# Optimization experiments

Measured on AMD Instinct MI355X. Metric: run time of the kernel, lower is better.

Reference implementation:

```python
import jax, jax.numpy as jnp
import numpy as np

D_MODEL = 1024
N_HEADS = 16
D_K = D_MODEL // N_HEADS
D_FF = 4096
EPS = 1e-5


def layer_norm(x, g, b):
    mu = jnp.mean(x, axis=-1, keepdims=True)
    var = jnp.var(x, axis=-1, keepdims=True)
    return (x - mu) * jax.lax.rsqrt(var + EPS) * g + b


def setup_inputs() -> dict:
    key = jax.random.key(0)
    ks = jax.random.split(key, 16)
    B, S = 4, 2048
    s_in = 1.0 / np.sqrt(D_MODEL)
    s_ff = 1.0 / np.sqrt(D_FF)
    return {
        "x": jax.random.normal(ks[0], (B, S, D_MODEL), jnp.float32),
        "mask": jnp.ones((B, 1, 1, S), jnp.int32),
        "Wq": jax.random.normal(ks[1], (D_MODEL, D_MODEL), jnp.float32) * s_in,
        "bq": jnp.zeros((D_MODEL,), jnp.float32),
        "Wk": jax.random.normal(ks[2], (D_MODEL, D_MODEL), jnp.float32) * s_in,
        "bk": jnp.zeros((D_MODEL,), jnp.float32),
        "Wv": jax.random.normal(ks[3], (D_MODEL, D_MODEL), jnp.float32) * s_in,
        "bv": jnp.zeros((D_MODEL,), jnp.float32),
        "Wo": jax.random.normal(ks[4], (D_MODEL, D_MODEL), jnp.float32) * s_in,
        "bo": jnp.zeros((D_MODEL,), jnp.float32),
        "W1": jax.random.normal(ks[5], (D_MODEL, D_FF), jnp.float32) * s_in,
        "b1": jnp.zeros((D_FF,), jnp.float32),
        "W2": jax.random.normal(ks[6], (D_FF, D_MODEL), jnp.float32) * s_ff,
        "b2": jnp.zeros((D_MODEL,), jnp.float32),
        "ln1_g": jnp.ones((D_MODEL,), jnp.float32),
        "ln1_b": jnp.zeros((D_MODEL,), jnp.float32),
        "ln2_g": jnp.ones((D_MODEL,), jnp.float32),
        "ln2_b": jnp.zeros((D_MODEL,), jnp.float32),
    }


def reference(x, mask, Wq, bq, Wk, bk, Wv, bv, Wo, bo, W1, b1, W2, b2,
              ln1_g, ln1_b, ln2_g, ln2_b):
    B, S, _ = x.shape
    h = layer_norm(x, ln1_g, ln1_b)  # norm1(x), used for q/k/v
    # project and split heads: [B,S,D] -> [B,H,S,Dk]
    def heads(t):
        return t.reshape(B, S, N_HEADS, D_K).transpose(0, 2, 1, 3)
    Q = heads(h @ Wq + bq)
    K = heads(h @ Wk + bk)
    V = heads(h @ Wv + bv)
    scores = jnp.einsum('bhqd,bhkd->bhqk', Q, K) / jnp.sqrt(jnp.float32(D_K))
    scores = jnp.where(mask == 0, jnp.float32(-1e9), scores)
    attn = jax.nn.softmax(scores, axis=-1)
    out = jnp.einsum('bhqk,bhkd->bhqd', attn, V)
    out = out.transpose(0, 2, 1, 3).reshape(B, S, D_MODEL)
    attn_out = out @ Wo + bo
    x = x + attn_out
    # FFN with pre-norm (torch nn.GELU default = exact erf gelu)
    h2 = layer_norm(x, ln2_g, ln2_b)
    ff = jax.nn.gelu(h2 @ W1 + b1, approximate=False) @ W2 + b2
    return x + ff
```

## Files before the change

kernel.cpp:

```cpp
#include <hip/hip_runtime.h>
#include <stdint.h>
#include <string.h>


typedef unsigned int       u32;
typedef unsigned short     u16;
typedef __bf16 bf16x8 __attribute__((ext_vector_type(8)));
typedef float  floatx4 __attribute__((ext_vector_type(4)));

#define D_MODEL 1024
#define N_HEADS 16
#define D_K     64
#define D_FF    4096
#define S_LEN   2048
#define N_TOK   8192
#define LDQKV   3072

__device__ __forceinline__ u16 f2b(float f) {
    u32 u = __float_as_uint(f);
    u32 r = (u + 0x7fffu + ((u >> 16) & 1u)) >> 16;
    return (u16)r;
}

__device__ __forceinline__ void gl_lds16(const void* g, void* l) {
    __builtin_amdgcn_global_load_lds(
        (const __attribute__((address_space(1))) u32*)g,
        (__attribute__((address_space(3))) u32*)l, 16, 0, 0);
}

__global__ __launch_bounds__(256) void transpose_bf16_kernel(
    const float* __restrict__ src, u16* __restrict__ dst, int R, int C)
{
    __shared__ float tile[32][33];
    int cb = blockIdx.x * 32, rb = blockIdx.y * 32;
    int tx = threadIdx.x & 31, ty = threadIdx.x >> 5;
    #pragma unroll
    for (int yy = ty; yy < 32; yy += 8)
        tile[yy][tx] = src[(size_t)(rb + yy) * C + cb + tx];
    __syncthreads();
    #pragma unroll
    for (int yy = ty; yy < 32; yy += 8)
        dst[(size_t)(cb + yy) * R + rb + tx] = f2b(tile[tx][yy]);
}

__global__ __launch_bounds__(256) void vt_kernel(
    const u16* __restrict__ Qkv, u16* __restrict__ Vt)
{
    __shared__ u32 tile[64 * 65];
    int b = blockIdx.z, h = blockIdx.y, s0 = blockIdx.x * 64;
    int t = threadIdx.x;
    int r = t >> 2, cg = (t & 3) * 16;
    const u16* src = &Qkv[((size_t)(b * S_LEN + s0 + r)) * LDQKV + 2048 + h * D_K + cg];
    uint4 a0 = *(const uint4*)src;
    uint4 a1 = *(const uint4*)(src + 8);
    u16 vals[16];
    memcpy(vals, &a0, 16); memcpy(vals + 8, &a1, 16);
    #pragma unroll
    for (int j = 0; j < 16; j++) tile[r * 65 + cg + j] = vals[j];
    __syncthreads();
    int f = t & 63, w = t >> 6;
    u16 outv[16];
    #pragma unroll
    for (int j = 0; j < 16; j++) outv[j] = (u16)tile[(w * 16 + j) * 65 + f];
    uint4 o0, o1; memcpy(&o0, outv, 16); memcpy(&o1, outv + 8, 16);
    u16* dst = &Vt[((size_t)((b * N_HEADS + h) * D_K + f)) * S_LEN + s0 + w * 16];
    *(uint4*)dst = o0; *(uint4*)(dst + 8) = o1;
}

__global__ __launch_bounds__(256) void ln_kernel(
    const float* __restrict__ x, const float* __restrict__ g,
    const float* __restrict__ b, u16* __restrict__ out)
{
    int row = blockIdx.x;
    int t = threadIdx.x;
    const float4* xr = reinterpret_cast<const float4*>(x + (size_t)row * D_MODEL);
    float4 v = xr[t];
    float s  = v.x + v.y + v.z + v.w;
    float ss = v.x * v.x + v.y * v.y + v.z * v.z + v.w * v.w;
    #pragma unroll
    for (int off = 32; off >= 1; off >>= 1) {
        s  += __shfl_down(s,  off);
        ss += __shfl_down(ss, off);
    }
    __shared__ float red[8];
    int wid = t >> 6, ln = t & 63;
    if (ln == 0) { red[wid] = s; red[4 + wid] = ss; }
    __syncthreads();
    float S  = red[0] + red[1] + red[2] + red[3];
    float SS = red[4] + red[5] + red[6] + red[7];
    float mu  = S * (1.0f / D_MODEL);
    float var = SS * (1.0f / D_MODEL) - mu * mu;
    float rs  = rsqrtf(var + 1e-5f);
    const float4* g4 = reinterpret_cast<const float4*>(g);
    const float4* b4 = reinterpret_cast<const float4*>(b);
    float4 gv = g4[t], bv = b4[t];
    float y0 = (v.x - mu) * rs * gv.x + bv.x;
    float y1 = (v.y - mu) * rs * gv.y + bv.y;
    float y2 = (v.z - mu) * rs * gv.z + bv.z;
    float y3 = (v.w - mu) * rs * gv.w + bv.w;
    uint2 pk;
    pk.x = (u32)f2b(y0) | ((u32)f2b(y1) << 16);
    pk.y = (u32)f2b(y2) | ((u32)f2b(y3) << 16);
    *reinterpret_cast<uint2*>(out + (size_t)row * D_MODEL + t * 4) = pk;
}

__global__ __launch_bounds__(256) void gemm_bt(
    const u16* __restrict__ A, const u16* __restrict__ Bt,
    const float* __restrict__ bias, const float* __restrict__ biasK,
    const float* __restrict__ biasV, const float* __restrict__ resid,
    float* __restrict__ outF, u16* __restrict__ outB,
    int M, int N, int K, int flags)
{
    __shared__ u16 As[128 * 32];
    __shared__ u16 Bs[128 * 32];
    int m0 = blockIdx.y * 128, n0 = blockIdx.x * 128;
    int t = threadIdx.x;
    int wave = t >> 6, lane = t & 63, quad = lane >> 4, lr = lane & 15;
    int wm = (wave >> 1) * 64, wn = (wave & 1) * 64;

    floatx4 acc[4][4] = {};

    int seg0 = t;
    int r0 = seg0 >> 2, c0 = (seg0 & 3) * 8;
    int seg1 = t + 256;
    int r1 = seg1 >> 2, c1 = (seg1 & 3) * 8;

    for (int k0 = 0; k0 < K; k0 += 32) {
        gl_lds16(&A [(size_t)(m0 + r0) * K + k0 + c0], &As[seg0 * 8]);
        gl_lds16(&A [(size_t)(m0 + r1) * K + k0 + c1], &As[seg1 * 8]);
        gl_lds16(&Bt[(size_t)(n0 + r0) * K + k0 + c0], &Bs[seg0 * 8]);
        gl_lds16(&Bt[(size_t)(n0 + r1) * K + k0 + c1], &Bs[seg1 * 8]);
        __syncthreads();

        bf16x8 af[4], bfr[4];
        #pragma unroll
        for (int mt = 0; mt < 4; mt++)
            af[mt] = *reinterpret_cast<const bf16x8*>(&As[(wm + mt * 16 + lr) * 32 + quad * 8]);
        #pragma unroll
        for (int nt = 0; nt < 4; nt++)
            bfr[nt] = *reinterpret_cast<const bf16x8*>(&Bs[(wn + nt * 16 + lr) * 32 + quad * 8]);
        #pragma unroll
        for (int mt = 0; mt < 4; mt++)
            #pragma unroll
            for (int nt = 0; nt < 4; nt++)
                acc[mt][nt] = __builtin_amdgcn_mfma_f32_16x16x32_bf16(
                    af[mt], bfr[nt], acc[mt][nt], 0, 0, 0);
        __syncthreads();
    }

    bool do_gelu = (flags & 1) != 0;
    #pragma unroll
    for (int mt = 0; mt < 4; mt++) {
        #pragma unroll
        for (int nt = 0; nt < 4; nt++) {
            int c = n0 + wn + nt * 16 + lr;
            float bsv;
            if (biasK) {
                if (c >= 2048)      bsv = biasV[c - 2048];
                else if (c >= 1024) bsv = biasK[c - 1024];
                else                bsv = bias[c];
            } else {
                bsv = bias[c];
            }
            #pragma unroll
            for (int i = 0; i < 4; i++) {
                int r = m0 + wm + mt * 16 + quad * 4 + i;
                float v = acc[mt][nt][i] + bsv;
                if (resid) v += resid[(size_t)r * N + c];
                if (do_gelu) v = 0.5f * v * (1.0f + erff(v * 0.70710678118654752f));
                if (outF) outF[(size_t)r * N + c] = v;
                if (outB) outB[(size_t)r * N + c] = f2b(v);
            }
        }
    }
}

__global__ __launch_bounds__(256, 4) void attn_mfma_kernel(
    const u16* __restrict__ Qkv, const u16* __restrict__ Vt,
    const int* __restrict__ mask, u16* __restrict__ ctx)
{
    __shared__ u16 Ks[64 * 72];
    __shared__ u16 Vs[64 * 72];
    __shared__ u16 Ps[128 * 72];
    __shared__ float Ms[64];

    int b = blockIdx.z, h = blockIdx.y;
    int q0 = blockIdx.x * 128;
    int t = threadIdx.x;
    int wave = t >> 6, lane = t & 63, quad = lane >> 4, lr = lane & 15;
    int wm = wave * 32;

    bf16x8 qf[2][2];
    #pragma unroll
    for (int mt = 0; mt < 2; mt++)
        #pragma unroll
        for (int kk = 0; kk < 2; kk++)
            qf[mt][kk] = *(const bf16x8*)&Qkv[((size_t)(b * S_LEN + q0 + wm + mt * 16 + lr)) * LDQKV
                                              + h * D_K + kk * 32 + quad * 8];

    floatx4 o[2][4] = {};
    float lsum[2][4] = {};
    const float scale = 0.125f;

    for (int kt = 0; kt < S_LEN / 64; kt++) {
        __syncthreads();
        {
            int row = t >> 2, cg = (t & 3) * 16;
            const u16* kg = &Qkv[((size_t)(b * S_LEN + kt * 64 + row)) * LDQKV + 1024 + h * D_K + cg];
            *(uint4*)&Ks[row * 72 + cg]     = *(const uint4*)kg;
            *(uint4*)&Ks[row * 72 + cg + 8] = *(const uint4*)(kg + 8);
            const u16* vg = &Vt[((size_t)((b * N_HEADS + h) * D_K + row)) * S_LEN + kt * 64 + cg];
            *(uint4*)&Vs[row * 72 + cg]     = *(const uint4*)vg;
            *(uint4*)&Vs[row * 72 + cg + 8] = *(const uint4*)(vg + 8);
            if (t < 64) Ms[t] = (mask[b * S_LEN + kt * 64 + t] == 0) ? -1e9f : 0.0f;
        }
        __syncthreads();

        floatx4 s[2][4] = {};
        #pragma unroll
        for (int kk = 0; kk < 2; kk++) {
            bf16x8 bk[4];
            #pragma unroll
            for (int n = 0; n < 4; n++)
                bk[n] = *(const bf16x8*)&Ks[(n * 16 + lr) * 72 + kk * 32 + quad * 8];
            #pragma unroll
            for (int mt = 0; mt < 2; mt++)
                #pragma unroll
                for (int n = 0; n < 4; n++)
                    s[mt][n] = __builtin_amdgcn_mfma_f32_16x16x32_bf16(
                        qf[mt][kk], bk[n], s[mt][n], 0, 0, 0);
        }

        #pragma unroll
        for (int mt = 0; mt < 2; mt++) {
            #pragma unroll
            for (int n = 0; n < 4; n++) {
                float msk = Ms[n * 16 + lr];
                #pragma unroll
                for (int i = 0; i < 4; i++) {
                    float p = __expf(s[mt][n][i] * scale + msk);
                    lsum[mt][i] += p;
                    Ps[(wm + mt * 16 + quad * 4 + i) * 72 + n * 16 + lr] = f2b(p);
                }
            }
        }

        bf16x8 bv[4][2];
        #pragma unroll
        for (int kk = 0; kk < 2; kk++)
            #pragma unroll
            for (int n = 0; n < 4; n++)
                bv[n][kk] = *(const bf16x8*)&Vs[(n * 16 + lr) * 72 + kk * 32 + quad * 8];

        __syncthreads();

        #pragma unroll
        for (int kk = 0; kk < 2; kk++) {
            #pragma unroll
            for (int mt = 0; mt < 2; mt++) {
                bf16x8 ap = *(const bf16x8*)&Ps[(wm + mt * 16 + lr) * 72 + kk * 32 + quad * 8];
                #pragma unroll
                for (int n = 0; n < 4; n++)
                    o[mt][n] = __builtin_amdgcn_mfma_f32_16x16x32_bf16(
                        ap, bv[n][kk], o[mt][n], 0, 0, 0);
            }
        }
    }

    #pragma unroll
    for (int mt = 0; mt < 2; mt++)
        #pragma unroll
        for (int i = 0; i < 4; i++) {
            float v = lsum[mt][i];
            v += __shfl_xor(v, 1);
            v += __shfl_xor(v, 2);
            v += __shfl_xor(v, 4);
            v += __shfl_xor(v, 8);
            lsum[mt][i] = 1.0f / v;
        }
    #pragma unroll
    for (int mt = 0; mt < 2; mt++)
        #pragma unroll
        for (int n = 0; n < 4; n++)
            #pragma unroll
            for (int i = 0; i < 4; i++) {
                int row = q0 + wm + mt * 16 + quad * 4 + i;
                int col = h * D_K + n * 16 + lr;
                ctx[((size_t)(b * S_LEN + row)) * D_MODEL + col] =
                    f2b(o[mt][n][i] * lsum[mt][i]);
            }
}

extern "C" void kernel_launch(void* const* d_in, const int* in_sizes, int n_in,
                              void* d_out, int out_size, void* d_ws, size_t ws_size,
                              hipStream_t stream)
{
    const float* x    = (const float*)d_in[0];
    const int*   mask = (const int*)  d_in[1];
    const float* Wq   = (const float*)d_in[2];
    const float* bq   = (const float*)d_in[3];
    const float* Wk   = (const float*)d_in[4];
    const float* bk   = (const float*)d_in[5];
    const float* Wv   = (const float*)d_in[6];
    const float* bv   = (const float*)d_in[7];
    const float* Wo   = (const float*)d_in[8];
    const float* bo   = (const float*)d_in[9];
    const float* W1   = (const float*)d_in[10];
    const float* b1   = (const float*)d_in[11];
    const float* W2   = (const float*)d_in[12];
    const float* b2   = (const float*)d_in[13];
    const float* ln1g = (const float*)d_in[14];
    const float* ln1b = (const float*)d_in[15];
    const float* ln2g = (const float*)d_in[16];
    const float* ln2b = (const float*)d_in[17];
    float* out = (float*)d_out;

    char* ws = (char*)d_ws;
    const size_t MB = 1u << 20;
    u16*   wqkvT = (u16*)(ws + 0 * MB);
    u16*   woT   = (u16*)(ws + 6 * MB);
    u16*   w1T   = (u16*)(ws + 8 * MB);
    u16*   w2T   = (u16*)(ws + 16 * MB);
    u16*   h     = (u16*)(ws + 24 * MB);
    u16*   Qkv   = (u16*)(ws + 40 * MB);
    u16*   ctx   = (u16*)(ws + 88 * MB);
    float* x1    = (float*)(ws + 104 * MB);
    u16*   Vt    = h;

    bool full = ws_size >= 216 * MB;
    u16* h2  = full ? (u16*)(ws + 136 * MB) : Qkv;
    u16* ff1 = full ? (u16*)(ws + 152 * MB) : (u16*)(ws + 56 * MB);
    int nchunk = full ? 1 : 2;
    int Mc = N_TOK / nchunk;

    dim3 blk(256);

    transpose_bf16_kernel<<<dim3(32, 32),  blk, 0, stream>>>(Wq, wqkvT,            1024, 1024);
    transpose_bf16_kernel<<<dim3(32, 32),  blk, 0, stream>>>(Wk, wqkvT + 1024*1024, 1024, 1024);
    transpose_bf16_kernel<<<dim3(32, 32),  blk, 0, stream>>>(Wv, wqkvT + 2048*1024, 1024, 1024);
    transpose_bf16_kernel<<<dim3(32, 32),  blk, 0, stream>>>(Wo, woT, 1024, 1024);
    transpose_bf16_kernel<<<dim3(128, 32), blk, 0, stream>>>(W1, w1T, 1024, 4096);
    transpose_bf16_kernel<<<dim3(32, 128), blk, 0, stream>>>(W2, w2T, 4096, 1024);

    ln_kernel<<<N_TOK, blk, 0, stream>>>(x, ln1g, ln1b, h);

    gemm_bt<<<dim3(24, 64), blk, 0, stream>>>(h, wqkvT, bq, bk, bv, nullptr,
                                              nullptr, Qkv, N_TOK, LDQKV, D_MODEL, 0);

    vt_kernel<<<dim3(32, 16, 4), blk, 0, stream>>>(Qkv, Vt);

    attn_mfma_kernel<<<dim3(16, 16, 4), blk, 0, stream>>>(Qkv, Vt, mask, ctx);

    gemm_bt<<<dim3(8, 64), blk, 0, stream>>>(ctx, woT, bo, nullptr, nullptr, x,
                                             x1, nullptr, N_TOK, D_MODEL, D_MODEL, 0);

    ln_kernel<<<N_TOK, blk, 0, stream>>>(x1, ln2g, ln2b, h2);

    for (int c = 0; c < nchunk; c++) {
        size_t ro = (size_t)c * Mc * D_MODEL;
        size_t rf = (size_t)c * Mc * D_FF;
        gemm_bt<<<dim3(32, Mc / 128), blk, 0, stream>>>(
            h2 + ro, w1T, b1, nullptr, nullptr, nullptr,
            nullptr, ff1 + (full ? rf : 0), Mc, D_FF, D_MODEL, 1);
        gemm_bt<<<dim3(8, Mc / 128), blk, 0, stream>>>(
            ff1 + (full ? rf : 0), w2T, b2, nullptr, nullptr, x1 + ro,
            out + ro, nullptr, Mc, D_MODEL, D_FF, 0);
    }
}
```

Measured before the change: 701.5 us.

## Split-K the FFN down-projection with atomics and XOR-swizzle GEMM LDS tiles

The W2 GEMM (K=4096) is split into 4 K-slices that accumulate into an output pre-initialised with the residual plus bias, using float atomicAdd. This raises the workgroup count for a GEMM that had only 512 tiles. Separately, the LDS tile layout in every GEMM is XOR-swizzled on the column group to cut bank conflicts on fragment reads. The atomics add global traffic and make the summation order nondeterministic, and an extra init kernel is launched.

```diff
diff --git a/kernel.cpp b/kernel.cpp
--- a/kernel.cpp
+++ b/kernel.cpp
@@ -104,12 +104,23 @@
     *reinterpret_cast<uint2*>(out + (size_t)row * D_MODEL + t * 4) = pk;
 }
 
+__global__ __launch_bounds__(256) void init_out_kernel(
+    const float* __restrict__ x1, const float* __restrict__ bias,
+    float* __restrict__ out)
+{
+    int row = blockIdx.x, t = threadIdx.x;
+    float4 v = reinterpret_cast<const float4*>(x1 + (size_t)row * D_MODEL)[t];
+    float4 b = reinterpret_cast<const float4*>(bias)[t];
+    v.x += b.x; v.y += b.y; v.z += b.z; v.w += b.w;
+    reinterpret_cast<float4*>(out + (size_t)row * D_MODEL)[t] = v;
+}
+
 __global__ __launch_bounds__(256) void gemm_bt(
     const u16* __restrict__ A, const u16* __restrict__ Bt,
     const float* __restrict__ bias, const float* __restrict__ biasK,
     const float* __restrict__ biasV, const float* __restrict__ resid,
     float* __restrict__ outF, u16* __restrict__ outB,
-    int M, int N, int K, int flags)
+    int M, int N, int K, int kslices, int flags)
 {
     __shared__ u16 As[128 * 32];
     __shared__ u16 Bs[128 * 32];
@@ -118,27 +129,29 @@
     int wave = t >> 6, lane = t & 63, quad = lane >> 4, lr = lane & 15;
     int wm = (wave >> 1) * 64, wn = (wave & 1) * 64;
 
+    int Klen = K / kslices;
+    int kbeg = blockIdx.z * Klen, kend = kbeg + Klen;
+
     floatx4 acc[4][4] = {};
 
-    int seg0 = t;
-    int r0 = seg0 >> 2, c0 = (seg0 & 3) * 8;
-    int seg1 = t + 256;
-    int r1 = seg1 >> 2, c1 = (seg1 & 3) * 8;
-
-    for (int k0 = 0; k0 < K; k0 += 32) {
-        gl_lds16(&A [(size_t)(m0 + r0) * K + k0 + c0], &As[seg0 * 8]);
-        gl_lds16(&A [(size_t)(m0 + r1) * K + k0 + c1], &As[seg1 * 8]);
-        gl_lds16(&Bt[(size_t)(n0 + r0) * K + k0 + c0], &Bs[seg0 * 8]);
-        gl_lds16(&Bt[(size_t)(n0 + r1) * K + k0 + c1], &Bs[seg1 * 8]);
+    int s0 = t,       r0 = s0 >> 2, g0 = ((s0 & 3) ^ ((r0 >> 1) & 3)) * 8;
+    int s1 = t + 256, r1 = s1 >> 2, g1 = ((s1 & 3) ^ ((r1 >> 1) & 3)) * 8;
+    int csw = (quad ^ ((lr >> 1) & 3)) * 8;
+
+    for (int k0 = kbeg; k0 < kend; k0 += 32) {
+        gl_lds16(&A [(size_t)(m0 + r0) * K + k0 + g0], &As[s0 * 8]);
+        gl_lds16(&A [(size_t)(m0 + r1) * K + k0 + g1], &As[s1 * 8]);
+        gl_lds16(&Bt[(size_t)(n0 + r0) * K + k0 + g0], &Bs[s0 * 8]);
+        gl_lds16(&Bt[(size_t)(n0 + r1) * K + k0 + g1], &Bs[s1 * 8]);
         __syncthreads();
 
         bf16x8 af[4], bfr[4];
         #pragma unroll
         for (int mt = 0; mt < 4; mt++)
-            af[mt] = *reinterpret_cast<const bf16x8*>(&As[(wm + mt * 16 + lr) * 32 + quad * 8]);
+            af[mt] = *reinterpret_cast<const bf16x8*>(&As[(wm + mt * 16 + lr) * 32 + csw]);
         #pragma unroll
         for (int nt = 0; nt < 4; nt++)
-            bfr[nt] = *reinterpret_cast<const bf16x8*>(&Bs[(wn + nt * 16 + lr) * 32 + quad * 8]);
+            bfr[nt] = *reinterpret_cast<const bf16x8*>(&Bs[(wn + nt * 16 + lr) * 32 + csw]);
         #pragma unroll
         for (int mt = 0; mt < 4; mt++)
             #pragma unroll
@@ -148,24 +161,32 @@
         __syncthreads();
     }
 
-    bool do_gelu = (flags & 1) != 0;
+    bool do_gelu  = (flags & 1) != 0;
+    bool do_atom  = (flags & 2) != 0;
     #pragma unroll
     for (int mt = 0; mt < 4; mt++) {
         #pragma unroll
         for (int nt = 0; nt < 4; nt++) {
             int c = n0 + wn + nt * 16 + lr;
-            float bsv;
-            if (biasK) {
-                if (c >= 2048)      bsv = biasV[c - 2048];
-                else if (c >= 1024) bsv = biasK[c - 1024];
-                else                bsv = bias[c];
-            } else {
-                bsv = bias[c];
+            float bsv = 0.0f;
+            if (!do_atom) {
+                if (biasK) {
+                    if (c >= 2048)      bsv = biasV[c - 2048];
+                    else if (c >= 1024) bsv = biasK[c - 1024];
+                    else                bsv = bias[c];
+                } else {
+                    bsv = bias[c];
+                }
             }
             #pragma unroll
             for (int i = 0; i < 4; i++) {
                 int r = m0 + wm + mt * 16 + quad * 4 + i;
-                float v = acc[mt][nt][i] + bsv;
+                float v = acc[mt][nt][i];
+                if (do_atom) {
+                    atomicAdd(&outF[(size_t)r * N + c], v);
+                    continue;
+                }
+                v += bsv;
                 if (resid) v += resid[(size_t)r * N + c];
                 if (do_gelu) v = 0.5f * v * (1.0f + erff(v * 0.70710678118654752f));
                 if (outF) outF[(size_t)r * N + c] = v;
@@ -335,7 +356,7 @@
 
     dim3 blk(256);
 
-    transpose_bf16_kernel<<<dim3(32, 32),  blk, 0, stream>>>(Wq, wqkvT,            1024, 1024);
+    transpose_bf16_kernel<<<dim3(32, 32),  blk, 0, stream>>>(Wq, wqkvT,             1024, 1024);
     transpose_bf16_kernel<<<dim3(32, 32),  blk, 0, stream>>>(Wk, wqkvT + 1024*1024, 1024, 1024);
     transpose_bf16_kernel<<<dim3(32, 32),  blk, 0, stream>>>(Wv, wqkvT + 2048*1024, 1024, 1024);
     transpose_bf16_kernel<<<dim3(32, 32),  blk, 0, stream>>>(Wo, woT, 1024, 1024);
@@ -345,14 +366,14 @@
     ln_kernel<<<N_TOK, blk, 0, stream>>>(x, ln1g, ln1b, h);
 
     gemm_bt<<<dim3(24, 64), blk, 0, stream>>>(h, wqkvT, bq, bk, bv, nullptr,
-                                              nullptr, Qkv, N_TOK, LDQKV, D_MODEL, 0);
+                                              nullptr, Qkv, N_TOK, LDQKV, D_MODEL, 1, 0);
 
     vt_kernel<<<dim3(32, 16, 4), blk, 0, stream>>>(Qkv, Vt);
 
     attn_mfma_kernel<<<dim3(16, 16, 4), blk, 0, stream>>>(Qkv, Vt, mask, ctx);
 
     gemm_bt<<<dim3(8, 64), blk, 0, stream>>>(ctx, woT, bo, nullptr, nullptr, x,
-                                             x1, nullptr, N_TOK, D_MODEL, D_MODEL, 0);
+                                             x1, nullptr, N_TOK, D_MODEL, D_MODEL, 1, 0);
 
     ln_kernel<<<N_TOK, blk, 0, stream>>>(x1, ln2g, ln2b, h2);
 
@@ -361,9 +382,10 @@
         size_t rf = (size_t)c * Mc * D_FF;
         gemm_bt<<<dim3(32, Mc / 128), blk, 0, stream>>>(
             h2 + ro, w1T, b1, nullptr, nullptr, nullptr,
-            nullptr, ff1 + (full ? rf : 0), Mc, D_FF, D_MODEL, 1);
-        gemm_bt<<<dim3(8, Mc / 128), blk, 0, stream>>>(
-            ff1 + (full ? rf : 0), w2T, b2, nullptr, nullptr, x1 + ro,
-            out + ro, nullptr, Mc, D_MODEL, D_FF, 0);
-    }
-}
+            nullptr, ff1 + (full ? rf : 0), Mc, D_FF, D_MODEL, 1, 1);
+        init_out_kernel<<<Mc, blk, 0, stream>>>(x1 + ro, b2, out + ro);
+        gemm_bt<<<dim3(8, Mc / 128, 4), blk, 0, stream>>>(
+            ff1 + (full ? rf : 0), w2T, nullptr, nullptr, nullptr, nullptr,
+            out + ro, nullptr, Mc, D_MODEL, D_FF, 4, 2);
+    }
+}
```

Measured after the change: 796.5 us. 13.5% more time.

## Swizzle GEMM LDS tiles and remap blocks into per-XCD row bands

Applied to the files above, without the earlier changes.

The GEMM now uses a flattened 1D grid. Each block index is remapped so that the blocks on each of the 8 XCDs cover a contiguous band of M rows, which should improve L2 reuse of the A tiles within an XCD. The LDS tile layout also gets an XOR swizzle on its 16-byte column groups, applied on the global-load side, and the fragment reads invert it. This is meant to reduce LDS bank conflicts. The mapping assumes M/128 is divisible by 8 and that hardware dispatches blocks round-robin across XCDs.

```diff
diff --git a/kernel.cpp b/kernel.cpp
--- a/kernel.cpp
+++ b/kernel.cpp
@@ -113,32 +113,38 @@
 {
     __shared__ u16 As[128 * 32];
     __shared__ u16 Bs[128 * 32];
-    int m0 = blockIdx.y * 128, n0 = blockIdx.x * 128;
+
+    int nbx = N >> 7, nby = M >> 7;
+    int bid = blockIdx.x;
+    int xcd = bid & 7, p = bid >> 3;
+    int bandsz = nby >> 3;
+    int m0 = (xcd * bandsz + p / nbx) * 128;
+    int n0 = (p % nbx) * 128;
+
     int t = threadIdx.x;
     int wave = t >> 6, lane = t & 63, quad = lane >> 4, lr = lane & 15;
     int wm = (wave >> 1) * 64, wn = (wave & 1) * 64;
 
     floatx4 acc[4][4] = {};
 
-    int seg0 = t;
-    int r0 = seg0 >> 2, c0 = (seg0 & 3) * 8;
-    int seg1 = t + 256;
-    int r1 = seg1 >> 2, c1 = (seg1 & 3) * 8;
+    int s0 = t,       r0 = s0 >> 2, g0 = ((s0 & 3) ^ ((r0 >> 1) & 3)) * 8;
+    int s1 = t + 256, r1 = s1 >> 2, g1 = ((s1 & 3) ^ ((r1 >> 1) & 3)) * 8;
+    int csw = (quad ^ ((lr >> 1) & 3)) * 8;
 
     for (int k0 = 0; k0 < K; k0 += 32) {
-        gl_lds16(&A [(size_t)(m0 + r0) * K + k0 + c0], &As[seg0 * 8]);
-        gl_lds16(&A [(size_t)(m0 + r1) * K + k0 + c1], &As[seg1 * 8]);
-        gl_lds16(&Bt[(size_t)(n0 + r0) * K + k0 + c0], &Bs[seg0 * 8]);
-        gl_lds16(&Bt[(size_t)(n0 + r1) * K + k0 + c1], &Bs[seg1 * 8]);
+        gl_lds16(&A [(size_t)(m0 + r0) * K + k0 + g0], &As[s0 * 8]);
+        gl_lds16(&A [(size_t)(m0 + r1) * K + k0 + g1], &As[s1 * 8]);
+        gl_lds16(&Bt[(size_t)(n0 + r0) * K + k0 + g0], &Bs[s0 * 8]);
+        gl_lds16(&Bt[(size_t)(n0 + r1) * K + k0 + g1], &Bs[s1 * 8]);
         __syncthreads();
 
         bf16x8 af[4], bfr[4];
         #pragma unroll
         for (int mt = 0; mt < 4; mt++)
-            af[mt] = *reinterpret_cast<const bf16x8*>(&As[(wm + mt * 16 + lr) * 32 + quad * 8]);
+            af[mt] = *reinterpret_cast<const bf16x8*>(&As[(wm + mt * 16 + lr) * 32 + csw]);
         #pragma unroll
         for (int nt = 0; nt < 4; nt++)
-            bfr[nt] = *reinterpret_cast<const bf16x8*>(&Bs[(wn + nt * 16 + lr) * 32 + quad * 8]);
+            bfr[nt] = *reinterpret_cast<const bf16x8*>(&Bs[(wn + nt * 16 + lr) * 32 + csw]);
         #pragma unroll
         for (int mt = 0; mt < 4; mt++)
             #pragma unroll
@@ -335,7 +341,7 @@
 
     dim3 blk(256);
 
-    transpose_bf16_kernel<<<dim3(32, 32),  blk, 0, stream>>>(Wq, wqkvT,            1024, 1024);
+    transpose_bf16_kernel<<<dim3(32, 32),  blk, 0, stream>>>(Wq, wqkvT,             1024, 1024);
     transpose_bf16_kernel<<<dim3(32, 32),  blk, 0, stream>>>(Wk, wqkvT + 1024*1024, 1024, 1024);
     transpose_bf16_kernel<<<dim3(32, 32),  blk, 0, stream>>>(Wv, wqkvT + 2048*1024, 1024, 1024);
     transpose_bf16_kernel<<<dim3(32, 32),  blk, 0, stream>>>(Wo, woT, 1024, 1024);
@@ -344,25 +350,25 @@
 
     ln_kernel<<<N_TOK, blk, 0, stream>>>(x, ln1g, ln1b, h);
 
-    gemm_bt<<<dim3(24, 64), blk, 0, stream>>>(h, wqkvT, bq, bk, bv, nullptr,
-                                              nullptr, Qkv, N_TOK, LDQKV, D_MODEL, 0);
+    gemm_bt<<<dim3(24 * 64), blk, 0, stream>>>(h, wqkvT, bq, bk, bv, nullptr,
+                                               nullptr, Qkv, N_TOK, LDQKV, D_MODEL, 0);
 
     vt_kernel<<<dim3(32, 16, 4), blk, 0, stream>>>(Qkv, Vt);
 
     attn_mfma_kernel<<<dim3(16, 16, 4), blk, 0, stream>>>(Qkv, Vt, mask, ctx);
 
-    gemm_bt<<<dim3(8, 64), blk, 0, stream>>>(ctx, woT, bo, nullptr, nullptr, x,
-                                             x1, nullptr, N_TOK, D_MODEL, D_MODEL, 0);
+    gemm_bt<<<dim3(8 * 64), blk, 0, stream>>>(ctx, woT, bo, nullptr, nullptr, x,
+                                              x1, nullptr, N_TOK, D_MODEL, D_MODEL, 0);
 
     ln_kernel<<<N_TOK, blk, 0, stream>>>(x1, ln2g, ln2b, h2);
 
     for (int c = 0; c < nchunk; c++) {
         size_t ro = (size_t)c * Mc * D_MODEL;
         size_t rf = (size_t)c * Mc * D_FF;
-        gemm_bt<<<dim3(32, Mc / 128), blk, 0, stream>>>(
+        gemm_bt<<<dim3(32 * (Mc / 128)), blk, 0, stream>>>(
             h2 + ro, w1T, b1, nullptr, nullptr, nullptr,
             nullptr, ff1 + (full ? rf : 0), Mc, D_FF, D_MODEL, 1);
-        gemm_bt<<<dim3(8, Mc / 128), blk, 0, stream>>>(
+        gemm_bt<<<dim3(8 * (Mc / 128)), blk, 0, stream>>>(
             ff1 + (full ? rf : 0), w2T, b2, nullptr, nullptr, x1 + ro,
             out + ro, nullptr, Mc, D_MODEL, D_FF, 0);
     }
```

Result: faster. 685.4 us (-2.3%).
